# Kernel tuning notes

Measured on AMD Instinct MI355X. Metric: run time of the kernel, lower is better.

## Reference

```python
import jax, jax.numpy as jnp
import numpy as np

LUMA, GPTS, FM = 8, 16, 8  # luma_bins, guide_pts, feature_multiplier
NIN, NOUT = 3, 3


def conv(x, w, b=None, stride=1, relu=True):
    k = w.shape[2]
    p = k // 2
    y = jax.lax.conv_general_dilated(x, w, (stride, stride), ((p, p), (p, p)),
                                     dimension_numbers=('NCHW', 'OIHW', 'NCHW'))
    if b is not None:
        y = y + b[None, :, None, None]
    return jax.nn.relu(y) if relu else y


def slice_grid(grid, guide):
    # grid: [B, C, L, gh, gw]; guide: [B, H, W] in [0,1]
    B, C, L, gh, gw = grid.shape
    _, H, W = guide.shape
    xs = (jnp.arange(W, dtype=jnp.float32) + 0.5) * gw / W - 0.5   # [W]
    ys = (jnp.arange(H, dtype=jnp.float32) + 0.5) * gh / H - 0.5   # [H]
    gz = guide * L - 0.5                                           # [B,H,W]
    fx, fy, fz = jnp.floor(xs), jnp.floor(ys), jnp.floor(gz)
    grid_flat = grid.reshape(B, C, L * gh * gw)
    out = jnp.zeros((B, C, H, W), dtype=grid.dtype)
    for dz in (0, 1):
        zi = jnp.clip(fz + dz, 0, L - 1).astype(jnp.int32)         # [B,H,W]
        wz = jnp.maximum(1.0 - jnp.abs(gz - (fz + dz)), 0.0)
        for dy in (0, 1):
            yi = jnp.clip(fy + dy, 0, gh - 1).astype(jnp.int32)    # [H]
            wy = jnp.maximum(1.0 - jnp.abs(ys - (fy + dy)), 0.0)
            for dx in (0, 1):
                xi = jnp.clip(fx + dx, 0, gw - 1).astype(jnp.int32)  # [W]
                wx = jnp.maximum(1.0 - jnp.abs(xs - (fx + dx)), 0.0)
                idx = (zi * gh + yi[None, :, None]) * gw + xi[None, None, :]  # [B,H,W]
                vals = jnp.take_along_axis(grid_flat, idx.reshape(B, 1, H * W), axis=2)
                vals = vals.reshape(B, C, H, W)
                w = (wz * wy[None, :, None] * wx[None, None, :])[:, None]      # [B,1,H,W]
                out = out + vals * w
    return out


def forward(image_lowres, image_fullres,
            sw0, sb0, sw1, sb1, sw2, sb2, sw3, sb3,
            gw0, gb0, gw1, gb1,
            fw0, fb0, fw1, fb1, fw2, fb2,
            lw0, lb0, lw1,
            pw, pb,
            ccm_w, ccm_b, shifts, slopes, proj_w, proj_b):
    B = image_lowres.shape[0]
    # splat: 4 stride-2 convs 256 -> 16
    x = conv(image_lowres, sw0, sb0, 2)
    x = conv(x, sw1, sb1, 2)
    x = conv(x, sw2, sb2, 2)
    x = conv(x, sw3, sb3, 2)                      # [B,64,16,16]
    # global path: 16 -> 8 -> 4, AdaptiveAvgPool2d(4) is identity at 4x4
    g = conv(x, gw0, gb0, 2)
    g = conv(g, gw1, gb1, 2)                      # [B,64,4,4]
    g = g.reshape(B, -1)                          # [B,1024]
    g = jax.nn.relu(g @ fw0.T + fb0)
    g = jax.nn.relu(g @ fw1.T + fb1)
    g = g @ fw2.T + fb2                           # [B,64]
    # local path
    loc = conv(x, lw0, lb0, 1)
    loc = conv(loc, lw1, None, 1, relu=False)     # [B,64,16,16]
    fusion = jax.nn.relu(g[:, :, None, None] + loc)
    co = conv(fusion, pw, pb, 1, relu=False)      # [B,96,16,16]
    gh_, gw_ = co.shape[2], co.shape[3]
    # split into LUMA chunks of 12 along channels, stack on dim 2
    grid = co.reshape(B, LUMA, NOUT * (NIN + 1), gh_, gw_).transpose(0, 2, 1, 3, 4)  # [B,12,8,16,16]
    # guidemap: ccm -> piecewise-linear curve -> projection -> hardtanh
    gm = conv(image_fullres, ccm_w, ccm_b, 1, relu=False)           # [B,3,H,W]
    sh = shifts.reshape(1, NIN, 1, 1, GPTS)
    gm = (slopes * jax.nn.relu(gm[..., None] - sh)).sum(axis=4)     # [B,3,H,W]
    gm = (proj_w.reshape(1, NIN, 1, 1) * gm).sum(axis=1) + proj_b[0]  # [B,H,W]
    gm = jnp.clip(gm, 0.0, 1.0)
    # bilateral slice with offset
    coeff = slice_grid(grid, gm)                                    # [B,12,H,W]
    H, W = image_fullres.shape[2], image_fullres.shape[3]
    coeff = coeff.reshape(B, NOUT, NIN + 1, H, W)
    out = jnp.einsum('boihw,bihw->bohw', coeff[:, :, :NIN], image_fullres) + coeff[:, :, NIN]
    return jnp.clip(out, 0.0, 1.0)  # eval-mode hardtanh


def setup_inputs() -> dict:
    key = jax.random.key(0)
    ks = iter(jax.random.split(key, 40))
    def cw(o, i, k):
        return (jax.random.normal(next(ks), (o, i, k, k), jnp.float32) / np.sqrt(i * k * k)).astype(jnp.float32)
    def fcw(o, i):
        return (jax.random.normal(next(ks), (o, i), jnp.float32) / np.sqrt(i)).astype(jnp.float32)
    z = lambda n: jnp.zeros((n,), jnp.float32)
    inp = {}
    inp['image_lowres'] = jax.random.uniform(next(ks), (2, 3, 256, 256), jnp.float32)
    inp['image_fullres'] = jax.random.uniform(next(ks), (2, 3, 1024, 1024), jnp.float32)
    # splat: channels 3->8->16->32->64
    inp['sw0'], inp['sb0'] = cw(8, 3, 3), z(8)
    inp['sw1'], inp['sb1'] = cw(16, 8, 3), z(16)
    inp['sw2'], inp['sb2'] = cw(32, 16, 3), z(32)
    inp['sw3'], inp['sb3'] = cw(64, 32, 3), z(64)
    # global convs (8*fm = 64)
    inp['gw0'], inp['gb0'] = cw(64, 64, 3), z(64)
    inp['gw1'], inp['gb1'] = cw(64, 64, 3), z(64)
    # global fc: 1024 -> 256 -> 128 -> 64
    inp['fw0'], inp['fb0'] = fcw(256, 1024), z(256)
    inp['fw1'], inp['fb1'] = fcw(128, 256), z(128)
    inp['fw2'], inp['fb2'] = fcw(64, 128), z(64)
    # local
    inp['lw0'], inp['lb0'] = cw(64, 64, 3), z(64)
    inp['lw1'] = cw(64, 64, 3)
    # prediction 1x1: 64 -> 96
    inp['pw'], inp['pb'] = cw(96, 64, 1), z(96)
    # guide params
    ccm = np.identity(3, dtype=np.float32) + np.float32(0.0001) * np.float32(np.random.RandomState(0).randn(1)[0])
    inp['ccm_w'] = jnp.asarray(ccm.reshape(3, 3, 1, 1))
    inp['ccm_b'] = z(3)
    shifts = np.linspace(0, 1, GPTS, endpoint=False, dtype=np.float32)
    inp['shifts'] = jnp.tile(jnp.asarray(shifts)[None, None, None, :], (3, 1, 1, 1))  # [3,1,1,16]
    slopes = np.zeros((1, 3, 1, 1, GPTS), dtype=np.float32); slopes[..., 0] = 1.0
    inp['slopes'] = jnp.asarray(slopes)
    inp['proj_w'] = jnp.ones((1, 3, 1, 1), jnp.float32) / 3.0
    inp['proj_b'] = z(1)
    return inp


def reference(image_lowres, image_fullres, sw0, sb0, sw1, sb1, sw2, sb2, sw3, sb3,
              gw0, gb0, gw1, gb1, fw0, fb0, fw1, fb1, fw2, fb2,
              lw0, lb0, lw1, pw, pb, ccm_w, ccm_b, shifts, slopes, proj_w, proj_b):
    return forward(image_lowres, image_fullres, sw0, sb0, sw1, sb1, sw2, sb2, sw3, sb3,
                   gw0, gb0, gw1, gb1, fw0, fb0, fw1, fb1, fw2, fb2,
                   lw0, lb0, lw1, pw, pb, ccm_w, ccm_b, shifts, slopes, proj_w, proj_b)
```

## Files before the change

kernel.cpp:

```cpp
#include <hip/hip_runtime.h>
#include <math.h>


static inline int cdiv(int a, int b) { return (a + b - 1) / b; }

__global__ __launch_bounds__(1024) void splat_k(
    const float* __restrict__ img,
    const float* __restrict__ w0, const float* __restrict__ b0,
    const float* __restrict__ w1, const float* __restrict__ b1,
    const float* __restrict__ w2, const float* __restrict__ b2,
    const float* __restrict__ w3, const float* __restrict__ b3,
    float* __restrict__ x3out, int B) {
    __shared__ float simg[3 * 47 * 48];
    __shared__ float s0[23 * 23 * 8];
    __shared__ float s1[11 * 11 * 16];
    __shared__ float s2[5 * 5 * 32];

    const int t  = threadIdx.x;
    const int b  = blockIdx.x >> 6;
    const int ty = (blockIdx.x >> 3) & 7;
    const int tx = blockIdx.x & 7;
    const int y0base = 16 * ty - 7, x0base = 16 * tx - 7;
    const int y1base = 8 * ty - 3,  x1base = 8 * tx - 3;
    const int y2base = 4 * ty - 1,  x2base = 4 * tx - 1;
    const int imgY0 = 32 * ty - 15, imgX0 = 32 * tx - 15;
    const float* ib = img + (size_t)b * 3 * 65536;

    for (int i = t; i < 3 * 47 * 47; i += 1024) {
        int xx = i % 47;
        int yy = (i / 47) % 47;
        int c  = i / (47 * 47);
        int y = imgY0 + yy, x = imgX0 + xx;
        float v = 0.0f;
        if (y >= 0 && y < 256 && x >= 0 && x < 256)
            v = ib[c * 65536 + y * 256 + x];
        simg[(c * 47 + yy) * 48 + xx] = v;
    }
    __syncthreads();

    for (int i = t; i < 23 * 23 * 8; i += 1024) {
        int c  = i & 7;
        int xx = (i >> 3) % 23;
        int yy = (i >> 3) / 23;
        int y = y0base + yy, x = x0base + xx;
        float acc = 0.0f;
        if (y >= 0 && y < 128 && x >= 0 && x < 128) {
            acc = b0[c];
            const float* wr = w0 + c * 27;
#pragma unroll
            for (int ci = 0; ci < 3; ++ci)
#pragma unroll
                for (int ky = 0; ky < 3; ++ky)
#pragma unroll
                    for (int kx = 0; kx < 3; ++kx)
                        acc += simg[(ci * 47 + 2 * yy + ky) * 48 + 2 * xx + kx]
                             * wr[ci * 9 + ky * 3 + kx];
            acc = fmaxf(acc, 0.0f);
        }
        s0[i] = acc;
    }
    __syncthreads();

    for (int i = t; i < 11 * 11 * 16; i += 1024) {
        int c  = i & 15;
        int xx = (i >> 4) % 11;
        int yy = (i >> 4) / 11;
        int y = y1base + yy, x = x1base + xx;
        float acc = 0.0f;
        if (y >= 0 && y < 64 && x >= 0 && x < 64) {
            acc = b1[c];
            const float* wr = w1 + c * 72;
            int l0y = 2 * yy;
            int l0x = 2 * xx;
            for (int ci = 0; ci < 8; ++ci)
#pragma unroll
                for (int ky = 0; ky < 3; ++ky)
#pragma unroll
                    for (int kx = 0; kx < 3; ++kx)
                        acc += s0[((l0y + ky) * 23 + (l0x + kx)) * 8 + ci] * wr[ci * 9 + ky * 3 + kx];
            acc = fmaxf(acc, 0.0f);
        }
        s1[i] = acc;
    }
    __syncthreads();

    if (t < 5 * 5 * 32) {
        int i = t;
        int c  = i & 31;
        int xx = (i >> 5) % 5;
        int yy = (i >> 5) / 5;
        int y = y2base + yy, x = x2base + xx;
        float acc = 0.0f;
        if (y >= 0 && y < 32 && x >= 0 && x < 32) {
            acc = b2[c];
            const float* wr = w2 + c * 144;
            int l1y = 2 * yy;
            int l1x = 2 * xx;
            for (int ci = 0; ci < 16; ++ci)
#pragma unroll
                for (int ky = 0; ky < 3; ++ky)
#pragma unroll
                    for (int kx = 0; kx < 3; ++kx)
                        acc += s1[((l1y + ky) * 11 + (l1x + kx)) * 16 + ci] * wr[ci * 9 + ky * 3 + kx];
            acc = fmaxf(acc, 0.0f);
        }
        s2[i] = acc;
    }
    __syncthreads();

    {
        int out  = t >> 2;
        int part = t & 3;
        int c  = out & 63;
        int xx = (out >> 6) & 1;
        int yy = out >> 7;
        int l2y = 2 * yy, l2x = 2 * xx;
        const float* wr = w3 + c * 288;
        float acc = 0.0f;
        for (int ci = part; ci < 32; ci += 4)
#pragma unroll
            for (int ky = 0; ky < 3; ++ky)
#pragma unroll
                for (int kx = 0; kx < 3; ++kx)
                    acc += s2[((l2y + ky) * 5 + (l2x + kx)) * 32 + ci] * wr[ci * 9 + ky * 3 + kx];
        acc += __shfl_xor(acc, 1);
        acc += __shfl_xor(acc, 2);
        if (part == 0) {
            int y = 2 * ty + yy, x = 2 * tx + xx;
            acc = fmaxf(acc + b3[c], 0.0f);
            x3out[((size_t)(b * 16 + y) * 16 + x) * 64 + c] = acc;
        }
    }
}


__device__ __forceinline__ void wave_conv_one(
    const float* __restrict__ in, const float* __restrict__ wgt,
    const float* __restrict__ bias, float* __restrict__ out,
    int B, int Cin, int Hin, int Win, int Cout, int Hout, int Wout,
    int stride, int relu, int out_chw, int wid, int lane) {
    int copw = (Cin == 64) ? 1 : 2;
    int cow  = Cout / copw;
    int ci   = lane & (Cin - 1);
    int cw = wid % cow;
    int wo = (wid / cow) % Wout;
    int ho = (wid / (cow * Wout)) % Hout;
    int b  = wid / (cow * Wout * Hout);
    int co = cw * copw + ((copw == 2) ? (lane >> 5) : 0);
    int hb = ho * stride - 1, wb = wo * stride - 1;
    const float* wp = wgt + ((size_t)co * Cin + ci) * 9;
    float acc = 0.0f;
#pragma unroll
    for (int ky = 0; ky < 3; ++ky) {
        int hi = hb + ky;
        if (hi < 0 || hi >= Hin) continue;
#pragma unroll
        for (int kx = 0; kx < 3; ++kx) {
            int wi = wb + kx;
            if (wi < 0 || wi >= Win) continue;
            acc += in[((size_t)(b * Hin + hi) * Win + wi) * Cin + ci] * wp[ky * 3 + kx];
        }
    }
    for (int m = 1; m < Cin; m <<= 1) acc += __shfl_xor(acc, m);
    if (ci == 0) {
        if (bias) acc += bias[co];
        if (relu) acc = fmaxf(acc, 0.0f);
        if (out_chw) out[((size_t)(b * Cout + co) * Hout + ho) * Wout + wo] = acc;
        else         out[((size_t)(b * Hout + ho) * Wout + wo) * Cout + co] = acc;
    }
}

__global__ void gl0_k(const float* __restrict__ x3,
                      const float* __restrict__ gw, const float* __restrict__ gb, float* __restrict__ g0,
                      const float* __restrict__ lw, const float* __restrict__ lb, float* __restrict__ loc0,
                      int B) {
    int tid = blockIdx.x * blockDim.x + threadIdx.x;
    int wid = tid >> 6, lane = threadIdx.x & 63;
    int ng = B * 64 * 8 * 8;
    int nl = B * 64 * 16 * 16;
    if (wid < ng)            wave_conv_one(x3, gw, gb, g0,  B, 64, 16, 16, 64, 8, 8,  2, 1, 0, wid, lane);
    else if (wid < ng + nl)  wave_conv_one(x3, lw, lb, loc0, B, 64, 16, 16, 64, 16, 16, 1, 1, 0, wid - ng, lane);
}

__global__ void gl1_k(const float* __restrict__ g0, const float* __restrict__ loc0,
                      const float* __restrict__ gw, const float* __restrict__ gb, float* __restrict__ g1,
                      const float* __restrict__ lw, float* __restrict__ loc1, int B) {
    int tid = blockIdx.x * blockDim.x + threadIdx.x;
    int wid = tid >> 6, lane = threadIdx.x & 63;
    int ng = B * 64 * 4 * 4;
    int nl = B * 64 * 16 * 16;
    if (wid < ng)            wave_conv_one(g0, gw, gb, g1,   B, 64, 8, 8,  64, 4, 4,  2, 1, 1, wid, lane);
    else if (wid < ng + nl)  wave_conv_one(loc0, lw, nullptr, loc1, B, 64, 16, 16, 64, 16, 16, 1, 0, 0, wid - ng, lane);
}

__global__ void fc0_k(const float* __restrict__ g1, const float* __restrict__ fw0,
                      const float* __restrict__ fb0, float* __restrict__ f0, int B) {
    int tid  = blockIdx.x * blockDim.x + threadIdx.x;
    int wid  = tid >> 6;
    int lane = threadIdx.x & 63;
    if (wid >= B * 256) return;
    int o = wid & 255, b = wid >> 8;
    const float* ip = g1 + (size_t)b * 1024;
    const float* wp = fw0 + (size_t)o * 1024;
    float acc = 0.0f;
    for (int j = lane; j < 1024; j += 64) acc += ip[j] * wp[j];
    for (int m = 1; m < 64; m <<= 1) acc += __shfl_xor(acc, m);
    if (lane == 0) f0[wid] = fmaxf(acc + fb0[o], 0.0f);
}

__global__ __launch_bounds__(512) void pred_k(
    const float* __restrict__ f0g,
    const float* __restrict__ fw1, const float* __restrict__ fb1,
    const float* __restrict__ fw2, const float* __restrict__ fb2,
    const float* __restrict__ loc1,
    const float* __restrict__ pw, const float* __restrict__ pb,
    float* __restrict__ sco) {
    __shared__ float s_f0[256];
    __shared__ float s_f1[128];
    __shared__ float s_f2[64];
    __shared__ float s_loc[64];

    const int t    = threadIdx.x;
    const int b    = blockIdx.x >> 8;
    const int cell = blockIdx.x & 255;
    const int wl   = t >> 6;
    const int lane = t & 63;

    if (t < 256) s_f0[t] = f0g[b * 256 + t];
    else if (t < 320) s_loc[t - 256] = loc1[((size_t)(b * 256 + cell)) * 64 + (t - 256)];
    __syncthreads();

    for (int o = wl; o < 128; o += 8) {
        const float* wp = fw1 + (size_t)o * 256;
        float acc = 0.0f;
#pragma unroll
        for (int j = 0; j < 4; ++j) acc += s_f0[lane + j * 64] * wp[lane + j * 64];
        for (int m = 1; m < 64; m <<= 1) acc += __shfl_xor(acc, m);
        if (lane == 0) s_f1[o] = fmaxf(acc + fb1[o], 0.0f);
    }
    __syncthreads();
    for (int o = wl; o < 64; o += 8) {
        const float* wp = fw2 + (size_t)o * 128;
        float acc = s_f1[lane] * wp[lane] + s_f1[lane + 64] * wp[lane + 64];
        for (int m = 1; m < 64; m <<= 1) acc += __shfl_xor(acc, m);
        if (lane == 0) s_f2[o] = acc + fb2[o];
    }
    __syncthreads();

    float act = fmaxf(s_f2[lane] + s_loc[lane], 0.0f);
    float* so = sco + (size_t)b * 24576 + (size_t)cell * 96;
    for (int c = wl; c < 96; c += 8) {
        float acc = pw[(size_t)c * 64 + lane] * act;
        for (int m = 1; m < 64; m <<= 1) acc += __shfl_xor(acc, m);
        if (lane == 0) so[c] = acc + pb[c];
    }
}

#define RSTRIDE 196
__global__ __launch_bounds__(256, 4) void apply_k(
    const float* __restrict__ img, const float* __restrict__ sco,
    const float* __restrict__ ccm_w, const float* __restrict__ ccm_b,
    const float* __restrict__ shifts, const float* __restrict__ slopes,
    const float* __restrict__ proj_w, const float* __restrict__ proj_b,
    float* __restrict__ out) {
    __shared__ __align__(16) float s_sco[4 * 96];
    __shared__ __align__(16) float s_R[32 * RSTRIDE];

    const int t   = threadIdx.x;
    const int b   = blockIdx.x >> 10;
    const int rem = blockIdx.x & 1023;
    const int ty  = rem >> 5;
    const int tx  = rem & 31;
    const int fy0 = (ty - 1) >> 1;
    const int fx0 = (tx - 1) >> 1;

    if (t < 96) {
        int cell = t / 24;
        int i4 = t % 24;
        int dy = cell >> 1, dx = cell & 1;
        int gy = min(max(fy0 + dy, 0), 15);
        int gx = min(max(fx0 + dx, 0), 15);
        float4 v = ((const float4*)(sco + ((size_t)b * 256 + gy * 16 + gx) * 96))[i4];
        ((float4*)(s_sco + cell * 96))[i4] = v;
    }
    __syncthreads();

    for (int idx = t; idx < 1536; idx += 256) {
        int q = idx % 24;
        int rowdx = idx / 24;
        int row = rowdx >> 1, dx = rowdx & 1;
        float ys = ((float)(ty * 32 + row) + 0.5f) * 0.015625f - 0.5f;
        float wy1 = ys - (float)fy0;
        float wy0 = 1.0f - wy1;
        float4 a0 = ((const float4*)(s_sco + dx * 96))[q];
        float4 a1 = ((const float4*)(s_sco + (2 + dx) * 96))[q];
        float4 v = make_float4(wy0 * a0.x + wy1 * a1.x, wy0 * a0.y + wy1 * a1.y,
                               wy0 * a0.z + wy1 * a1.z, wy0 * a0.w + wy1 * a1.w);
        ((float4*)(s_R + row * RSTRIDE + dx * 96))[q] = v;
    }
    __syncthreads();

    const size_t plane = 1024 * 1024;
    const float* ibase = img + (size_t)b * 3 * plane;
    float* obase = out + (size_t)b * 3 * plane;

    const int row = t >> 3;
    const int xg  = (t & 7) * 4;
    const int y = ty * 32 + row;
    const int x0 = tx * 32 + xg;
    const size_t off = (size_t)y * 1024 + x0;

    float4 r4 = *(const float4*)(ibase + off);
    float4 g4 = *(const float4*)(ibase + plane + off);
    float4 b4 = *(const float4*)(ibase + 2 * plane + off);
    const float rj[4] = { r4.x, r4.y, r4.z, r4.w };
    const float gj[4] = { g4.x, g4.y, g4.z, g4.w };
    const float bj[4] = { b4.x, b4.y, b4.z, b4.w };

    const float* Rrow = s_R + row * RSTRIDE;
    float o_r[4], o_g[4], o_b[4];

#pragma unroll
    for (int j = 0; j < 4; ++j) {
        float r = rj[j], g = gj[j], bl = bj[j];

        float gd = proj_b[0];
#pragma unroll
        for (int c = 0; c < 3; ++c) {
            float v = ccm_b[c] + ccm_w[c * 3 + 0] * r + ccm_w[c * 3 + 1] * g + ccm_w[c * 3 + 2] * bl;
            float acc = 0.0f;
#pragma unroll
            for (int p = 0; p < 16; ++p)
                acc += slopes[c * 16 + p] * fmaxf(v - shifts[c * 16 + p], 0.0f);
            gd += proj_w[c] * acc;
        }
        gd = fminf(fmaxf(gd, 0.0f), 1.0f);

        float xs = ((float)(x0 + j) + 0.5f) * 0.015625f - 0.5f;
        float wx1 = xs - (float)fx0;
        float wx0 = 1.0f - wx1;
        float gz = gd * 8.0f - 0.5f;
        float fzf = floorf(gz);
        int fz = (int)fzf;
        float wz1 = gz - fzf;
        float wz0 = 1.0f - wz1;

        float ar = 0.0f, ag = 0.0f, ab = 0.0f;
#pragma unroll
        for (int dz = 0; dz < 2; ++dz) {
            int zi = min(max(fz + dz, 0), 7);
            float wz = dz ? wz1 : wz0;
#pragma unroll
            for (int dx = 0; dx < 2; ++dx) {
                float wt = wz * (dx ? wx1 : wx0);
                const float4* gp = (const float4*)(Rrow + dx * 96 + zi * 12);
                float4 a0 = gp[0], a1 = gp[1], a2 = gp[2];
                ar += wt * (a0.x * r + a0.y * g + a0.z * bl + a0.w);
                ag += wt * (a1.x * r + a1.y * g + a1.z * bl + a1.w);
                ab += wt * (a2.x * r + a2.y * g + a2.z * bl + a2.w);
            }
        }
        o_r[j] = fminf(fmaxf(ar, 0.0f), 1.0f);
        o_g[j] = fminf(fmaxf(ag, 0.0f), 1.0f);
        o_b[j] = fminf(fmaxf(ab, 0.0f), 1.0f);
    }

    *(float4*)(obase + off)             = make_float4(o_r[0], o_r[1], o_r[2], o_r[3]);
    *(float4*)(obase + plane + off)     = make_float4(o_g[0], o_g[1], o_g[2], o_g[3]);
    *(float4*)(obase + 2 * plane + off) = make_float4(o_b[0], o_b[1], o_b[2], o_b[3]);
}


extern "C" void kernel_launch(void* const* d_in, const int* in_sizes, int n_in,
                              void* d_out, int out_size, void* d_ws, size_t ws_size,
                              hipStream_t stream) {
    const float* img_lo = (const float*)d_in[0];
    const float* img_fr = (const float*)d_in[1];
    const float* sw0 = (const float*)d_in[2];  const float* sb0 = (const float*)d_in[3];
    const float* sw1 = (const float*)d_in[4];  const float* sb1 = (const float*)d_in[5];
    const float* sw2 = (const float*)d_in[6];  const float* sb2 = (const float*)d_in[7];
    const float* sw3 = (const float*)d_in[8];  const float* sb3 = (const float*)d_in[9];
    const float* gw0 = (const float*)d_in[10]; const float* gb0 = (const float*)d_in[11];
    const float* gw1 = (const float*)d_in[12]; const float* gb1 = (const float*)d_in[13];
    const float* fw0 = (const float*)d_in[14]; const float* fb0 = (const float*)d_in[15];
    const float* fw1 = (const float*)d_in[16]; const float* fb1 = (const float*)d_in[17];
    const float* fw2 = (const float*)d_in[18]; const float* fb2 = (const float*)d_in[19];
    const float* lw0 = (const float*)d_in[20]; const float* lb0 = (const float*)d_in[21];
    const float* lw1 = (const float*)d_in[22];
    const float* pw  = (const float*)d_in[23]; const float* pb  = (const float*)d_in[24];
    const float* ccm_w  = (const float*)d_in[25]; const float* ccm_b = (const float*)d_in[26];
    const float* shifts = (const float*)d_in[27];
    const float* slopes = (const float*)d_in[28];
    const float* proj_w = (const float*)d_in[29];
    const float* proj_b = (const float*)d_in[30];
    float* out = (float*)d_out;

    const int B = in_sizes[0] / (3 * 256 * 256);

    float* ws = (float*)d_ws;
    float* x3   = ws;
    float* g0   = x3 + (size_t)B * 64 * 16 * 16;
    float* g1   = g0 + (size_t)B * 64 * 8 * 8;
    float* f0   = g1 + (size_t)B * 64 * 4 * 4;
    float* loc0 = f0 + (size_t)B * 256;
    float* loc1 = loc0 + (size_t)B * 64 * 16 * 16;
    float* sco  = loc1 + (size_t)B * 64 * 16 * 16;

    const int T = 256;

    splat_k<<<B * 64, 1024, 0, stream>>>(img_lo, sw0, sb0, sw1, sb1, sw2, sb2, sw3, sb3, x3, B);
    {
        int nwaves = B * 64 * 8 * 8 + B * 64 * 16 * 16;
        gl0_k<<<cdiv(nwaves * 64, T), T, 0, stream>>>(x3, gw0, gb0, g0, lw0, lb0, loc0, B);
    }
    {
        int nwaves = B * 64 * 4 * 4 + B * 64 * 16 * 16;
        gl1_k<<<cdiv(nwaves * 64, T), T, 0, stream>>>(g0, loc0, gw1, gb1, g1, lw1, loc1, B);
    }
    fc0_k<<<cdiv(B * 256 * 64, T), T, 0, stream>>>(g1, fw0, fb0, f0, B);
    pred_k<<<B * 256, 512, 0, stream>>>(f0, fw1, fb1, fw2, fb2, loc1, pw, pb, sco);
    apply_k<<<B * 1024, 256, 0, stream>>>(img_fr, sco, ccm_w, ccm_b, shifts, slopes,
                                          proj_w, proj_b, out);
}
```

Before: 120.1 us.

## Fuse global conv1 and fc0 into local conv kernel launch

Merges the second global stride-2 conv, the first fully-connected layer, and the local 3x3 conv into one launch. Each global block recomputes the full 4x4x64 g1 tensor into shared memory, then computes a 32-output slice of fc0. This removes one kernel launch and the g1 round trip through global memory. In exchange, the g1 conv is computed redundantly eight times per batch element, and the launch now uses 1024-thread blocks.

```diff
diff --git a/kernel.cpp b/kernel.cpp
--- a/kernel.cpp
+++ b/kernel.cpp
@@ -182,30 +182,58 @@
     else if (wid < ng + nl)  wave_conv_one(x3, lw, lb, loc0, B, 64, 16, 16, 64, 16, 16, 1, 1, 0, wid - ng, lane);
 }
 
-__global__ void gl1_k(const float* __restrict__ g0, const float* __restrict__ loc0,
-                      const float* __restrict__ gw, const float* __restrict__ gb, float* __restrict__ g1,
-                      const float* __restrict__ lw, float* __restrict__ loc1, int B) {
-    int tid = blockIdx.x * blockDim.x + threadIdx.x;
-    int wid = tid >> 6, lane = threadIdx.x & 63;
-    int ng = B * 64 * 4 * 4;
-    int nl = B * 64 * 16 * 16;
-    if (wid < ng)            wave_conv_one(g0, gw, gb, g1,   B, 64, 8, 8,  64, 4, 4,  2, 1, 1, wid, lane);
-    else if (wid < ng + nl)  wave_conv_one(loc0, lw, nullptr, loc1, B, 64, 16, 16, 64, 16, 16, 1, 0, 0, wid - ng, lane);
-}
-
-__global__ void fc0_k(const float* __restrict__ g1, const float* __restrict__ fw0,
-                      const float* __restrict__ fb0, float* __restrict__ f0, int B) {
-    int tid  = blockIdx.x * blockDim.x + threadIdx.x;
-    int wid  = tid >> 6;
-    int lane = threadIdx.x & 63;
-    if (wid >= B * 256) return;
-    int o = wid & 255, b = wid >> 8;
-    const float* ip = g1 + (size_t)b * 1024;
-    const float* wp = fw0 + (size_t)o * 1024;
-    float acc = 0.0f;
-    for (int j = lane; j < 1024; j += 64) acc += ip[j] * wp[j];
-    for (int m = 1; m < 64; m <<= 1) acc += __shfl_xor(acc, m);
-    if (lane == 0) f0[wid] = fmaxf(acc + fb0[o], 0.0f);
+__global__ __launch_bounds__(1024) void glf_k(
+    const float* __restrict__ g0, const float* __restrict__ gw1, const float* __restrict__ gb1,
+    const float* __restrict__ fw0, const float* __restrict__ fb0, float* __restrict__ f0,
+    const float* __restrict__ loc0, const float* __restrict__ lw1, float* __restrict__ loc1,
+    int B) {
+    const int t    = threadIdx.x;
+    const int w    = t >> 6;
+    const int lane = t & 63;
+    const int GFCB = B * 8;
+
+    if ((int)blockIdx.x < GFCB) {
+        __shared__ float s_g1[1024];
+        const int b    = blockIdx.x >> 3;
+        const int part = blockIdx.x & 7;
+
+        for (int i = 0; i < 64; ++i) {
+            int o1 = w * 64 + i;
+            int co = o1 >> 4, ho = (o1 >> 2) & 3, wo = o1 & 3;
+            int hb = 2 * ho - 1, wb = 2 * wo - 1;
+            const float* wr = gw1 + ((size_t)co * 64 + lane) * 9;
+            float acc = 0.0f;
+#pragma unroll
+            for (int ky = 0; ky < 3; ++ky) {
+                int hi = hb + ky;
+                if (hi < 0 || hi >= 8) continue;
+#pragma unroll
+                for (int kx = 0; kx < 3; ++kx) {
+                    int wi = wb + kx;
+                    if (wi < 0 || wi >= 8) continue;
+                    acc += g0[((size_t)(b * 8 + hi) * 8 + wi) * 64 + lane] * wr[ky * 3 + kx];
+                }
+            }
+            for (int m = 1; m < 64; m <<= 1) acc += __shfl_xor(acc, m);
+            if (lane == 0) s_g1[o1] = fmaxf(acc + gb1[co], 0.0f);
+        }
+        __syncthreads();
+
+        for (int o2 = w; o2 < 32; o2 += 16) {
+            int o = part * 32 + o2;
+            const float* wp = fw0 + (size_t)o * 1024;
+            float acc = 0.0f;
+#pragma unroll
+            for (int m2 = 0; m2 < 16; ++m2) acc += s_g1[lane + m2 * 64] * wp[lane + m2 * 64];
+            for (int m = 1; m < 64; m <<= 1) acc += __shfl_xor(acc, m);
+            if (lane == 0) f0[b * 256 + o] = fmaxf(acc + fb0[o], 0.0f);
+        }
+    } else {
+        int wid = (blockIdx.x - GFCB) * 16 + w;
+        int nl = B * 64 * 16 * 16;
+        if (wid < nl)
+            wave_conv_one(loc0, lw1, nullptr, loc1, B, 64, 16, 16, 64, 16, 16, 1, 0, 0, wid, lane);
+    }
 }
 
 __global__ __launch_bounds__(512) void pred_k(
@@ -400,8 +428,7 @@
     float* ws = (float*)d_ws;
     float* x3   = ws;
     float* g0   = x3 + (size_t)B * 64 * 16 * 16;
-    float* g1   = g0 + (size_t)B * 64 * 8 * 8;
-    float* f0   = g1 + (size_t)B * 64 * 4 * 4;
+    float* f0   = g0 + (size_t)B * 64 * 8 * 8;
     float* loc0 = f0 + (size_t)B * 256;
     float* loc1 = loc0 + (size_t)B * 64 * 16 * 16;
     float* sco  = loc1 + (size_t)B * 64 * 16 * 16;
@@ -414,10 +441,9 @@
         gl0_k<<<cdiv(nwaves * 64, T), T, 0, stream>>>(x3, gw0, gb0, g0, lw0, lb0, loc0, B);
     }
     {
-        int nwaves = B * 64 * 4 * 4 + B * 64 * 16 * 16;
-        gl1_k<<<cdiv(nwaves * 64, T), T, 0, stream>>>(g0, loc0, gw1, gb1, g1, lw1, loc1, B);
-    }
-    fc0_k<<<cdiv(B * 256 * 64, T), T, 0, stream>>>(g1, fw0, fb0, f0, B);
+        int nblocks = B * 8 + cdiv(B * 64 * 16 * 16, 16);
+        glf_k<<<nblocks, 1024, 0, stream>>>(g0, gw1, gb1, fw0, fb0, f0, loc0, lw1, loc1, B);
+    }
     pred_k<<<B * 256, 512, 0, stream>>>(f0, fw1, fb1, fw2, fb2, loc1, pw, pb, sco);
     apply_k<<<B * 1024, 256, 0, stream>>>(img_fr, sco, ccm_w, ccm_b, shifts, slopes,
                                           proj_w, proj_b, out);
```

After: 174.1 us (median of 2 runs). 45.0% more time.

## Fuse fc0 into prediction kernel and process four cells per block

Applied to the files above, without the earlier changes.

Removes the separate fc0 kernel launch by computing the 1024->256 global FC inside the prediction kernel, redundantly in each block. Each 1024-thread block now handles four grid cells instead of one, which cuts the number of redundant fc1/fc2 evaluations by four. The cost is that every block re-reads the 256x1024 fw0 weights (mostly L2 hits) and repeats that FC, trading recomputation for one less launch and less intermediate global traffic.

```diff
diff --git a/kernel.cpp b/kernel.cpp
--- a/kernel.cpp
+++ b/kernel.cpp
@@ -193,44 +193,38 @@
     else if (wid < ng + nl)  wave_conv_one(loc0, lw, nullptr, loc1, B, 64, 16, 16, 64, 16, 16, 1, 0, 0, wid - ng, lane);
 }
 
-__global__ void fc0_k(const float* __restrict__ g1, const float* __restrict__ fw0,
-                      const float* __restrict__ fb0, float* __restrict__ f0, int B) {
-    int tid  = blockIdx.x * blockDim.x + threadIdx.x;
-    int wid  = tid >> 6;
-    int lane = threadIdx.x & 63;
-    if (wid >= B * 256) return;
-    int o = wid & 255, b = wid >> 8;
-    const float* ip = g1 + (size_t)b * 1024;
-    const float* wp = fw0 + (size_t)o * 1024;
-    float acc = 0.0f;
-    for (int j = lane; j < 1024; j += 64) acc += ip[j] * wp[j];
-    for (int m = 1; m < 64; m <<= 1) acc += __shfl_xor(acc, m);
-    if (lane == 0) f0[wid] = fmaxf(acc + fb0[o], 0.0f);
-}
-
-__global__ __launch_bounds__(512) void pred_k(
-    const float* __restrict__ f0g,
+__global__ __launch_bounds__(1024) void predf_k(
+    const float* __restrict__ g1g,
+    const float* __restrict__ fw0, const float* __restrict__ fb0,
     const float* __restrict__ fw1, const float* __restrict__ fb1,
     const float* __restrict__ fw2, const float* __restrict__ fb2,
     const float* __restrict__ loc1,
     const float* __restrict__ pw, const float* __restrict__ pb,
     float* __restrict__ sco) {
+    __shared__ float s_g1[1024];
     __shared__ float s_f0[256];
     __shared__ float s_f1[128];
     __shared__ float s_f2[64];
-    __shared__ float s_loc[64];
+    __shared__ float s_act[4 * 64];
 
     const int t    = threadIdx.x;
-    const int b    = blockIdx.x >> 8;
-    const int cell = blockIdx.x & 255;
-    const int wl   = t >> 6;
+    const int w    = t >> 6;
     const int lane = t & 63;
-
-    if (t < 256) s_f0[t] = f0g[b * 256 + t];
-    else if (t < 320) s_loc[t - 256] = loc1[((size_t)(b * 256 + cell)) * 64 + (t - 256)];
-    __syncthreads();
-
-    for (int o = wl; o < 128; o += 8) {
+    const int b    = blockIdx.x >> 6;
+    const int part = blockIdx.x & 63;
+
+    s_g1[t] = g1g[b * 1024 + t];
+    __syncthreads();
+
+    for (int o = w; o < 256; o += 16) {
+        const float* wp = fw0 + (size_t)o * 1024;
+        float acc = 0.0f;
+        for (int j = lane; j < 1024; j += 64) acc += s_g1[j] * wp[j];
+        for (int m = 1; m < 64; m <<= 1) acc += __shfl_xor(acc, m);
+        if (lane == 0) s_f0[o] = fmaxf(acc + fb0[o], 0.0f);
+    }
+    __syncthreads();
+    for (int o = w; o < 128; o += 16) {
         const float* wp = fw1 + (size_t)o * 256;
         float acc = 0.0f;
 #pragma unroll
@@ -239,7 +233,7 @@
         if (lane == 0) s_f1[o] = fmaxf(acc + fb1[o], 0.0f);
     }
     __syncthreads();
-    for (int o = wl; o < 64; o += 8) {
+    for (int o = w; o < 64; o += 16) {
         const float* wp = fw2 + (size_t)o * 128;
         float acc = s_f1[lane] * wp[lane] + s_f1[lane + 64] * wp[lane + 64];
         for (int m = 1; m < 64; m <<= 1) acc += __shfl_xor(acc, m);
@@ -247,12 +241,17 @@
     }
     __syncthreads();
 
-    float act = fmaxf(s_f2[lane] + s_loc[lane], 0.0f);
-    float* so = sco + (size_t)b * 24576 + (size_t)cell * 96;
-    for (int c = wl; c < 96; c += 8) {
-        float acc = pw[(size_t)c * 64 + lane] * act;
+    if (t < 256) {
+        int cell = t >> 6, i = t & 63;
+        s_act[t] = fmaxf(s_f2[i] + loc1[((size_t)(b * 256 + part * 4 + cell)) * 64 + i], 0.0f);
+    }
+    __syncthreads();
+
+    for (int v = w; v < 384; v += 16) {
+        int cell = v / 96, c = v % 96;
+        float acc = pw[(size_t)c * 64 + lane] * s_act[cell * 64 + lane];
         for (int m = 1; m < 64; m <<= 1) acc += __shfl_xor(acc, m);
-        if (lane == 0) so[c] = acc + pb[c];
+        if (lane == 0) sco[(size_t)b * 24576 + (size_t)(part * 4 + cell) * 96 + c] = acc + pb[c];
     }
 }
 
@@ -401,8 +400,7 @@
     float* x3   = ws;
     float* g0   = x3 + (size_t)B * 64 * 16 * 16;
     float* g1   = g0 + (size_t)B * 64 * 8 * 8;
-    float* f0   = g1 + (size_t)B * 64 * 4 * 4;
-    float* loc0 = f0 + (size_t)B * 256;
+    float* loc0 = g1 + (size_t)B * 64 * 4 * 4;
     float* loc1 = loc0 + (size_t)B * 64 * 16 * 16;
     float* sco  = loc1 + (size_t)B * 64 * 16 * 16;
 
@@ -417,8 +415,7 @@
         int nwaves = B * 64 * 4 * 4 + B * 64 * 16 * 16;
         gl1_k<<<cdiv(nwaves * 64, T), T, 0, stream>>>(g0, loc0, gw1, gb1, g1, lw1, loc1, B);
     }
-    fc0_k<<<cdiv(B * 256 * 64, T), T, 0, stream>>>(g1, fw0, fb0, f0, B);
-    pred_k<<<B * 256, 512, 0, stream>>>(f0, fw1, fb1, fw2, fb2, loc1, pw, pb, sco);
+    predf_k<<<B * 64, 1024, 0, stream>>>(g1, fw0, fb0, fw1, fb1, fw2, fb2, loc1, pw, pb, sco);
     apply_k<<<B * 1024, 256, 0, stream>>>(img_fr, sco, ccm_w, ccm_b, shifts, slopes,
                                           proj_w, proj_b, out);
 }
```

New measurement: 194.8 us. 62.2% more time.
